# Kernel optimization log

Hardware: AMD Instinct MI355X
Metric: run time of the kernel (lower is better)

## Reference

```python
import jax, jax.numpy as jnp
import numpy as np

NUM_USERS = 100_000
NUM_ITEMS = 50_000
EMBED_DIM = 64
NUM_LAYERS = 3
NUM_BASE_EDGES = 2_000_000
BATCH = 4096


def setup_inputs() -> dict:
    key = jax.random.key(0)
    k_ue, k_ie, k_u, k_i, k_uid, k_iid = jax.random.split(key, 6)
    N = NUM_USERS + NUM_ITEMS
    # learned embedding tables (std=0.01 init as in the torch module)
    user_emb = 0.01 * jax.random.normal(k_ue, (NUM_USERS, EMBED_DIM), dtype=jnp.float32)
    item_emb = 0.01 * jax.random.normal(k_ie, (NUM_ITEMS, EMBED_DIM), dtype=jnp.float32)
    # random bipartite interaction edges (u, v); symmetrized as in _build_graph
    u = jax.random.randint(k_u, (NUM_BASE_EDGES,), 0, NUM_USERS, dtype=jnp.int32)
    v = jax.random.randint(k_i, (NUM_BASE_EDGES,), 0, NUM_ITEMS, dtype=jnp.int32) + NUM_USERS
    rows = jnp.concatenate([u, v])  # [2E]
    cols = jnp.concatenate([v, u])  # [2E]
    # symmetric degree normalization: A_hat[r,c] = 1 / (sqrt(deg[r]) * sqrt(deg[c]))
    deg = jax.ops.segment_sum(jnp.ones_like(rows, dtype=jnp.float32), rows, num_segments=N)
    sqrt_deg = jnp.sqrt(deg)
    vals = 1.0 / (sqrt_deg[rows] * sqrt_deg[cols])
    user_ids = jax.random.randint(k_uid, (BATCH,), 0, NUM_USERS, dtype=jnp.int32)
    item_ids = jax.random.randint(k_iid, (BATCH,), 0, NUM_ITEMS, dtype=jnp.int32)
    return {
        "user_emb": user_emb,
        "item_emb": item_emb,
        "vals": vals,
        "rows": rows,
        "cols": cols,
        "user_ids": user_ids,
        "item_ids": item_ids,
    }


def _spmm(vals, rows, cols, x, num_segments):
    # COO SpMM: out[r] += vals[e] * x[cols[e]]  (irregular gather + scatter-add)
    return jax.ops.segment_sum(vals[:, None] * x[cols], rows, num_segments=num_segments)


def reference(user_emb, item_emb, vals, rows, cols, user_ids, item_ids):
    num_users = user_emb.shape[0]
    N = num_users + item_emb.shape[0]
    all_emb = jnp.concatenate([user_emb, item_emb], axis=0)  # [N, D]
    acc = jnp.zeros_like(all_emb)
    for _ in range(NUM_LAYERS):  # eval mode: no stochastic noise injection
        all_emb = _spmm(vals, rows, cols, all_emb, N)
        acc = acc + all_emb
    final = acc / NUM_LAYERS  # mean over layer outputs
    u = final[user_ids]                       # [B, D]
    i = final[item_ids + num_users]           # [B, D]
    return (u * i).sum(axis=-1)               # [B]
```

## Files before the change

### kernel.cpp

```cpp
#include <hip/hip_runtime.h>


#define EMBED_DIM 64
#define NUM_LAYERS 3
#define RSHIFT 8
#define RMASK 255
#define NBMAX 640
#define CAPU 8192
#define CAPI 12288
#define TP 7168
#define OUT_CAP 12288

__device__ __forceinline__ int bucket_base(int b, int BSPLIT) {
    int lo = (b < BSPLIT) ? b : BSPLIT;
    int hi = (b > BSPLIT) ? (b - BSPLIT) : 0;
    return lo * CAPU + hi * CAPI;
}


__device__ __forceinline__ unsigned bf16pair(float a, float b) {
    unsigned ia = __float_as_uint(a);
    unsigned ib = __float_as_uint(b);
    ia = (ia + 0x7fffu + ((ia >> 16) & 1u)) >> 16;
    ib = (ib + 0x7fffu + ((ib >> 16) & 1u)) & 0xffff0000u;
    return ia | ib;
}
__device__ __forceinline__ float bf_lo(unsigned u) { return __uint_as_float(u << 16); }
__device__ __forceinline__ float bf_hi(unsigned u) { return __uint_as_float(u & 0xffff0000u); }


__global__ __launch_bounds__(1024) void split_kernel(const int* __restrict__ uu,
                                                     const int* __restrict__ vv,
                                                     int* __restrict__ gcur,
                                                     int* __restrict__ bin, int E2, int NB,
                                                     int BSPLIT) {
    __shared__ int h[NBMAX], exl[NBMAX], curb[NBMAX], gb[NBMAX];
    __shared__ int wp[16];
    __shared__ int stage[2 * TP];
    int tid = threadIdx.x;
    int lane = tid & 63, wid = tid >> 6;
    for (int i = tid; i < NB; i += 1024) h[i] = 0;
    __syncthreads();
    int e0 = blockIdx.x * TP, e1 = min(e0 + TP, E2);
    int j = e0 + tid * 4;
    for (; j + 3 < e1; j += 4096) {
        int4 u4 = *(const int4*)(uu + j);
        int4 v4 = *(const int4*)(vv + j);
        atomicAdd(&h[u4.x >> RSHIFT], 1); atomicAdd(&h[v4.x >> RSHIFT], 1);
        atomicAdd(&h[u4.y >> RSHIFT], 1); atomicAdd(&h[v4.y >> RSHIFT], 1);
        atomicAdd(&h[u4.z >> RSHIFT], 1); atomicAdd(&h[v4.z >> RSHIFT], 1);
        atomicAdd(&h[u4.w >> RSHIFT], 1); atomicAdd(&h[v4.w >> RSHIFT], 1);
    }
    for (; j < e1; ++j) {
        atomicAdd(&h[uu[j] >> RSHIFT], 1);
        atomicAdd(&h[vv[j] >> RSHIFT], 1);
    }
    __syncthreads();
    {
        int v0 = (tid < NB) ? h[tid] : 0;
        int x = v0;
        for (int off = 1; off < 64; off <<= 1) {
            int y = __shfl_up(x, off, 64);
            if (lane >= off) x += y;
        }
        if (lane == 63) wp[wid] = x;
        __syncthreads();
        int wadd = 0;
        for (int k = 0; k < wid; ++k) wadd += wp[k];
        if (tid < NB) exl[tid] = wadd + x - v0;
        __syncthreads();
    }
    for (int b = tid; b < NB; b += 1024) {
        curb[b] = exl[b];
        gb[b]   = h[b] ? (bucket_base(b, BSPLIT) + atomicAdd(&gcur[b], h[b])) : 0;
    }
    __syncthreads();
    j = e0 + tid * 4;
    for (; j + 3 < e1; j += 4096) {
        int4 u4 = *(const int4*)(uu + j);
        int4 v4 = *(const int4*)(vv + j);
        int p;
        p = atomicAdd(&curb[u4.x >> RSHIFT], 1); stage[p] = (v4.x << RSHIFT) | (u4.x & RMASK);
        p = atomicAdd(&curb[v4.x >> RSHIFT], 1); stage[p] = (u4.x << RSHIFT) | (v4.x & RMASK);
        p = atomicAdd(&curb[u4.y >> RSHIFT], 1); stage[p] = (v4.y << RSHIFT) | (u4.y & RMASK);
        p = atomicAdd(&curb[v4.y >> RSHIFT], 1); stage[p] = (u4.y << RSHIFT) | (v4.y & RMASK);
        p = atomicAdd(&curb[u4.z >> RSHIFT], 1); stage[p] = (v4.z << RSHIFT) | (u4.z & RMASK);
        p = atomicAdd(&curb[v4.z >> RSHIFT], 1); stage[p] = (u4.z << RSHIFT) | (v4.z & RMASK);
        p = atomicAdd(&curb[u4.w >> RSHIFT], 1); stage[p] = (v4.w << RSHIFT) | (u4.w & RMASK);
        p = atomicAdd(&curb[v4.w >> RSHIFT], 1); stage[p] = (u4.w << RSHIFT) | (v4.w & RMASK);
    }
    for (; j < e1; ++j) {
        int u = uu[j], v = vv[j];
        int p1 = atomicAdd(&curb[u >> RSHIFT], 1);
        stage[p1] = (v << RSHIFT) | (u & RMASK);
        int p2 = atomicAdd(&curb[v >> RSHIFT], 1);
        stage[p2] = (u << RSHIFT) | (v & RMASK);
    }
    __syncthreads();
    int noct = tid >> 3, osub = tid & 7;
    for (int b = noct; b < NB; b += 128) {
        int cnt_b = h[b];
        int st = exl[b], g = gb[b];
        for (int k = osub; k < cnt_b; k += 8) bin[g + k] = stage[st + k];
    }
}


__global__ __launch_bounds__(1024) void csr_kernel(const int* __restrict__ bin,
                                                   const int* __restrict__ gcur,
                                                   int2* __restrict__ rpd,
                                                   int* __restrict__ col_idx,
                                                   const float4* __restrict__ ue,
                                                   const float4* __restrict__ ie,
                                                   unsigned* __restrict__ w0x,
                                                   int N, int U, int BSPLIT, int NB) {
    __shared__ int h2[256], cur2[256];
    __shared__ float rs2[256];
    __shared__ int wp[16];
    __shared__ __align__(16) int outst[OUT_CAP];
    int nbi = NB - BSPLIT;
    int bb  = blockIdx.x;
    int b   = (bb < nbi) ? (BSPLIT + bb) : (bb - nbi);
    int tid = threadIdx.x;
    int lane = tid & 63, wid = tid >> 6;
    int s = bucket_base(b, BSPLIT);
    int cnt = gcur[b];
    if (tid < 256) h2[tid] = 0;
    __syncthreads();
    int cnt4 = cnt >> 2;
    const int4* bin4 = (const int4*)(bin + s);
    for (int j = tid; j < cnt4; j += 1024) {
        int4 v = bin4[j];
        atomicAdd(&h2[v.x & RMASK], 1);
        atomicAdd(&h2[v.y & RMASK], 1);
        atomicAdd(&h2[v.z & RMASK], 1);
        atomicAdd(&h2[v.w & RMASK], 1);
    }
    for (int j = (cnt4 << 2) + tid; j < cnt; j += 1024) atomicAdd(&h2[bin[s + j] & RMASK], 1);
    __syncthreads();
    int myh = (tid < 256) ? h2[tid] : 0;
    if (tid < 256) rs2[tid] = (myh > 0) ? rsqrtf((float)myh) : 0.0f;
    {
        int x = myh;
        for (int off = 1; off < 64; off <<= 1) {
            int y = __shfl_up(x, off, 64);
            if (lane >= off) x += y;
        }
        if (lane == 63) wp[wid] = x;
        __syncthreads();
        if (tid < 256) {
            int wadd = 0;
            for (int k = 0; k < wid; ++k) wadd += wp[k];
            cur2[tid] = wadd + x - myh;
        }
    }
    int gr = (b << RSHIFT) + tid;
    if (tid < 256 && gr < N) {
        int2 v; v.x = s + cur2[tid]; v.y = myh;
        rpd[gr] = v;
    }
    __syncthreads();
    if (cnt <= OUT_CAP) {
        for (int j = tid; j < cnt4; j += 1024) {
            int4 v = bin4[j];
            int p;
            p = atomicAdd(&cur2[v.x & RMASK], 1); outst[p] = v.x >> RSHIFT;
            p = atomicAdd(&cur2[v.y & RMASK], 1); outst[p] = v.y >> RSHIFT;
            p = atomicAdd(&cur2[v.z & RMASK], 1); outst[p] = v.z >> RSHIFT;
            p = atomicAdd(&cur2[v.w & RMASK], 1); outst[p] = v.w >> RSHIFT;
        }
        for (int j = (cnt4 << 2) + tid; j < cnt; j += 1024) {
            int v = bin[s + j];
            int p = atomicAdd(&cur2[v & RMASK], 1);
            outst[p] = v >> RSHIFT;
        }
        __syncthreads();
        int4* dst4 = (int4*)(col_idx + s);
        for (int j = tid; j < cnt4; j += 1024) dst4[j] = ((const int4*)outst)[j];
        for (int j = (cnt4 << 2) + tid; j < cnt; j += 1024) col_idx[s + j] = outst[j];
    } else {
        for (int j = tid; j < cnt; j += 1024) {
            int v = bin[s + j];
            int p = atomicAdd(&cur2[v & RMASK], 1);
            col_idx[s + p] = v >> RSHIFT;
        }
    }
    for (int idx = tid; idx < 256 * 16; idx += 1024) {
        int rl = idx >> 4, sub = idx & 15;
        int n = (b << RSHIFT) + rl;
        if (n < N) {
            float4 v = (n < U) ? ue[(size_t)n * 16 + sub] : ie[(size_t)(n - U) * 16 + sub];
            float rs = rs2[rl];
            uint2 o;
            o.x = bf16pair(v.x * rs, v.y * rs);
            o.y = bf16pair(v.z * rs, v.w * rs);
            ((uint2*)w0x)[(size_t)n * 16 + sub] = o;
        }
    }
}


__global__ __launch_bounds__(256) void spmm_kernel(const int2* __restrict__ rpd,
                                                   const int* __restrict__ col_idx,
                                                   const uint4* __restrict__ x4,
                                                   uint4* __restrict__ y4, int N) {
    int gw   = (blockIdx.x * blockDim.x + threadIdx.x) >> 6;
    int lane = threadIdx.x & 63;
    int oct  = lane >> 3, sub = lane & 7;
    int r = gw * 8 + oct;
    if (r >= N) return;
    int2 rd = rpd[r];
    int s = rd.x;
    int d = rd.y;
    float2 a0 = {0, 0}, a1 = {0, 0}, a2 = {0, 0}, a3 = {0, 0};
    int k = 0;
    for (; k + 3 < d; k += 4) {
        int c0 = col_idx[s + k];
        int c1 = col_idx[s + k + 1];
        int c2 = col_idx[s + k + 2];
        int c3 = col_idx[s + k + 3];
        uint4 u0 = x4[(size_t)c0 * 8 + sub];
        uint4 u1 = x4[(size_t)c1 * 8 + sub];
        uint4 u2 = x4[(size_t)c2 * 8 + sub];
        uint4 u3 = x4[(size_t)c3 * 8 + sub];
        a0.x += bf_lo(u0.x); a0.y += bf_hi(u0.x);
        a1.x += bf_lo(u0.y); a1.y += bf_hi(u0.y);
        a2.x += bf_lo(u0.z); a2.y += bf_hi(u0.z);
        a3.x += bf_lo(u0.w); a3.y += bf_hi(u0.w);
        a0.x += bf_lo(u1.x); a0.y += bf_hi(u1.x);
        a1.x += bf_lo(u1.y); a1.y += bf_hi(u1.y);
        a2.x += bf_lo(u1.z); a2.y += bf_hi(u1.z);
        a3.x += bf_lo(u1.w); a3.y += bf_hi(u1.w);
        a0.x += bf_lo(u2.x); a0.y += bf_hi(u2.x);
        a1.x += bf_lo(u2.y); a1.y += bf_hi(u2.y);
        a2.x += bf_lo(u2.z); a2.y += bf_hi(u2.z);
        a3.x += bf_lo(u2.w); a3.y += bf_hi(u2.w);
        a0.x += bf_lo(u3.x); a0.y += bf_hi(u3.x);
        a1.x += bf_lo(u3.y); a1.y += bf_hi(u3.y);
        a2.x += bf_lo(u3.z); a2.y += bf_hi(u3.z);
        a3.x += bf_lo(u3.w); a3.y += bf_hi(u3.w);
    }
    for (; k < d; ++k) {
        int c0 = col_idx[s + k];
        uint4 u0 = x4[(size_t)c0 * 8 + sub];
        a0.x += bf_lo(u0.x); a0.y += bf_hi(u0.x);
        a1.x += bf_lo(u0.y); a1.y += bf_hi(u0.y);
        a2.x += bf_lo(u0.z); a2.y += bf_hi(u0.z);
        a3.x += bf_lo(u0.w); a3.y += bf_hi(u0.w);
    }
    float inv = (d > 0) ? (1.0f / (float)d) : 0.0f;
    uint4 o;
    o.x = bf16pair(a0.x * inv, a0.y * inv);
    o.y = bf16pair(a1.x * inv, a1.y * inv);
    o.z = bf16pair(a2.x * inv, a2.y * inv);
    o.w = bf16pair(a3.x * inv, a3.y * inv);
    y4[(size_t)r * 8 + sub] = o;
}


__global__ __launch_bounds__(128) void batch_readout_kernel(const int2* __restrict__ rpd,
                                                            const int* __restrict__ col_idx,
                                                            const uint4* __restrict__ x4,
                                                            const uint4* __restrict__ l1,
                                                            const uint4* __restrict__ l2,
                                                            const int* __restrict__ user_ids,
                                                            const int* __restrict__ item_ids,
                                                            float* __restrict__ out,
                                                            int B, int U) {
    __shared__ float sm[8][8][8];
    __shared__ float dsm[8];
    int tid = threadIdx.x;
    int oct = tid >> 3, sub = tid & 7;
    int pair = oct & 7, is_item = oct >> 3;
    int b = blockIdx.x * 8 + pair;
    bool active = (b < B);
    float sv[8];
#pragma unroll
    for (int k = 0; k < 8; ++k) sv[k] = 0.0f;
    float dd = 0.0f;
    if (active) {
        int r = is_item ? (item_ids[b] + U) : user_ids[b];
        int2 rd = rpd[r];
        int s = rd.x;
        int d = rd.y;
        dd = (float)d;
        float2 a0 = {0, 0}, a1 = {0, 0}, a2 = {0, 0}, a3 = {0, 0};
        int k = 0;
        for (; k + 3 < d; k += 4) {
            int c0 = col_idx[s + k];
            int c1 = col_idx[s + k + 1];
            int c2 = col_idx[s + k + 2];
            int c3 = col_idx[s + k + 3];
            uint4 u0 = x4[(size_t)c0 * 8 + sub];
            uint4 u1 = x4[(size_t)c1 * 8 + sub];
            uint4 u2 = x4[(size_t)c2 * 8 + sub];
            uint4 u3 = x4[(size_t)c3 * 8 + sub];
            a0.x += bf_lo(u0.x); a0.y += bf_hi(u0.x);
            a1.x += bf_lo(u0.y); a1.y += bf_hi(u0.y);
            a2.x += bf_lo(u0.z); a2.y += bf_hi(u0.z);
            a3.x += bf_lo(u0.w); a3.y += bf_hi(u0.w);
            a0.x += bf_lo(u1.x); a0.y += bf_hi(u1.x);
            a1.x += bf_lo(u1.y); a1.y += bf_hi(u1.y);
            a2.x += bf_lo(u1.z); a2.y += bf_hi(u1.z);
            a3.x += bf_lo(u1.w); a3.y += bf_hi(u1.w);
            a0.x += bf_lo(u2.x); a0.y += bf_hi(u2.x);
            a1.x += bf_lo(u2.y); a1.y += bf_hi(u2.y);
            a2.x += bf_lo(u2.z); a2.y += bf_hi(u2.z);
            a3.x += bf_lo(u2.w); a3.y += bf_hi(u2.w);
            a0.x += bf_lo(u3.x); a0.y += bf_hi(u3.x);
            a1.x += bf_lo(u3.y); a1.y += bf_hi(u3.y);
            a2.x += bf_lo(u3.z); a2.y += bf_hi(u3.z);
            a3.x += bf_lo(u3.w); a3.y += bf_hi(u3.w);
        }
        for (; k < d; ++k) {
            int c0 = col_idx[s + k];
            uint4 u0 = x4[(size_t)c0 * 8 + sub];
            a0.x += bf_lo(u0.x); a0.y += bf_hi(u0.x);
            a1.x += bf_lo(u0.y); a1.y += bf_hi(u0.y);
            a2.x += bf_lo(u0.z); a2.y += bf_hi(u0.z);
            a3.x += bf_lo(u0.w); a3.y += bf_hi(u0.w);
        }
        float inv = (d > 0) ? (1.0f / (float)d) : 0.0f;
        uint4 u1v = l1[(size_t)r * 8 + sub];
        uint4 u2v = l2[(size_t)r * 8 + sub];
        sv[0] = bf_lo(u1v.x) + bf_lo(u2v.x) + a0.x * inv;
        sv[1] = bf_hi(u1v.x) + bf_hi(u2v.x) + a0.y * inv;
        sv[2] = bf_lo(u1v.y) + bf_lo(u2v.y) + a1.x * inv;
        sv[3] = bf_hi(u1v.y) + bf_hi(u2v.y) + a1.y * inv;
        sv[4] = bf_lo(u1v.z) + bf_lo(u2v.z) + a2.x * inv;
        sv[5] = bf_hi(u1v.z) + bf_hi(u2v.z) + a2.y * inv;
        sv[6] = bf_lo(u1v.w) + bf_lo(u2v.w) + a3.x * inv;
        sv[7] = bf_hi(u1v.w) + bf_hi(u2v.w) + a3.y * inv;
    }
    if (is_item) {
#pragma unroll
        for (int k = 0; k < 8; ++k) sm[pair][sub][k] = sv[k];
        if (sub == 0) dsm[pair] = dd;
    }
    __syncthreads();
    if (!is_item && active) {
        float p = 0.0f;
#pragma unroll
        for (int k = 0; k < 8; ++k) p += sv[k] * sm[pair][sub][k];
#pragma unroll
        for (int off = 4; off > 0; off >>= 1) p += __shfl_down(p, off, 8);
        if (sub == 0) {
            float du = dd;
            float di = dsm[pair];
            out[b] = p * sqrtf(du) * sqrtf(di) * (1.0f / (NUM_LAYERS * NUM_LAYERS));
        }
    }
}


extern "C" void kernel_launch(void* const* d_in, const int* in_sizes, int n_in,
                              void* d_out, int out_size, void* d_ws, size_t ws_size,
                              hipStream_t stream) {
    const float* user_emb = (const float*)d_in[0];
    const float* item_emb = (const float*)d_in[1];
    const int*   rows     = (const int*)d_in[3];
    const int*   cols     = (const int*)d_in[4];
    const int*   user_ids = (const int*)d_in[5];
    const int*   item_ids = (const int*)d_in[6];
    float*       out      = (float*)d_out;

    const int U = in_sizes[0] / EMBED_DIM;
    const int I = in_sizes[1] / EMBED_DIM;
    const int E2 = in_sizes[3] >> 1;
    const int B = in_sizes[5];
    const int N = U + I;
    const int NB = (N + RMASK) >> RSHIFT;
    const int BSPLIT = U >> RSHIFT;

    const long long TOT = (long long)((NB < BSPLIT ? NB : BSPLIT)) * CAPU +
                          (long long)((NB > BSPLIT) ? (NB - BSPLIT) : 0) * CAPI;

    char* w = (char*)d_ws;
    unsigned* x2      = (unsigned*)w; w += (size_t)N * 32 * sizeof(unsigned);
    unsigned* L1      = (unsigned*)w; w += (size_t)N * 32 * sizeof(unsigned);
    unsigned* L2      = (unsigned*)w; w += (size_t)N * 32 * sizeof(unsigned);
    int*      bin     = (int*)w;      w += (size_t)TOT * sizeof(int);
    int*      col_idx = (int*)w;      w += (size_t)TOT * sizeof(int);
    int2*     rpd     = (int2*)w;     w += (size_t)N * sizeof(int2);
    int*      gcur    = (int*)w;      w += (size_t)NB * sizeof(int);

    const int GP = (E2 + TP - 1) / TP;

    hipMemsetAsync(gcur, 0, (size_t)NB * sizeof(int), stream);
    split_kernel<<<GP, 1024, 0, stream>>>(rows, cols, gcur, bin, E2, NB, BSPLIT);
    csr_kernel<<<NB, 1024, 0, stream>>>(bin, gcur, rpd, col_idx,
                                        (const float4*)user_emb, (const float4*)item_emb,
                                        x2, N, U, BSPLIT, NB);

    const int T = 256;
    const int GS = (N * 8 + T - 1) / T;
    spmm_kernel<<<GS, T, 0, stream>>>(rpd, col_idx, (const uint4*)x2, (uint4*)L1, N);
    spmm_kernel<<<GS, T, 0, stream>>>(rpd, col_idx, (const uint4*)L1, (uint4*)L2, N);

    batch_readout_kernel<<<(B + 7) / 8, 128, 0, stream>>>(rpd, col_idx,
                                                          (const uint4*)L2,
                                                          (const uint4*)L1, (const uint4*)L2,
                                                          user_ids, item_ids, out, B, U);
}
```

Measured before the change: 283.7 us.

## Split bf16 embedding tables into two 64-byte column halves for SpMM gathers

Stores each layer's bf16 embeddings as two separate half-width arrays (32 dims each, 64 bytes per row) instead of one 128-byte row. The SpMM kernel now assigns 4 lanes per row per half and interleaves blocks across the two halves, so each pass gathers from a table half the size, which should make the working set fit better in cache. The trade-off is that every col_idx is read twice (once per half), and rows from the two halves are handled by different blocks.

```diff
diff --git a/kernel.cpp b/kernel.cpp
--- a/kernel.cpp
+++ b/kernel.cpp
@@ -112,7 +112,8 @@
                                                    int* __restrict__ col_idx,
                                                    const float4* __restrict__ ue,
                                                    const float4* __restrict__ ie,
-                                                   unsigned* __restrict__ w0x,
+                                                   unsigned* __restrict__ w0a,
+                                                   unsigned* __restrict__ w0b,
                                                    int N, int U, int BSPLIT, int NB) {
     __shared__ int h2[256], cur2[256];
     __shared__ float rs2[256];
@@ -194,7 +195,8 @@
             uint2 o;
             o.x = bf16pair(v.x * rs, v.y * rs);
             o.y = bf16pair(v.z * rs, v.w * rs);
-            ((uint2*)w0x)[(size_t)n * 16 + sub] = o;
+            unsigned* dst = (sub < 8) ? w0a : w0b;
+            ((uint2*)dst)[(size_t)n * 8 + (sub & 7)] = o;
         }
     }
 }
@@ -202,13 +204,19 @@
 
 __global__ __launch_bounds__(256) void spmm_kernel(const int2* __restrict__ rpd,
                                                    const int* __restrict__ col_idx,
-                                                   const uint4* __restrict__ x4,
-                                                   uint4* __restrict__ y4, int N) {
-    int gw   = (blockIdx.x * blockDim.x + threadIdx.x) >> 6;
-    int lane = threadIdx.x & 63;
-    int oct  = lane >> 3, sub = lane & 7;
-    int r = gw * 8 + oct;
+                                                   const uint4* __restrict__ xa,
+                                                   const uint4* __restrict__ xb,
+                                                   uint4* __restrict__ ya,
+                                                   uint4* __restrict__ yb, int N) {
+    int bid = blockIdx.x;
+    int xm = bid & 7, jm = bid >> 3;
+    int half = xm >> 2;
+    int gidx = jm * 4 + (xm & 3);
+    int quad = threadIdx.x >> 2, sub = threadIdx.x & 3;
+    int r = gidx * 64 + quad;
     if (r >= N) return;
+    const uint4* xs = half ? xb : xa;
+    uint4*       ys = half ? yb : ya;
     int2 rd = rpd[r];
     int s = rd.x;
     int d = rd.y;
@@ -219,10 +227,10 @@
         int c1 = col_idx[s + k + 1];
         int c2 = col_idx[s + k + 2];
         int c3 = col_idx[s + k + 3];
-        uint4 u0 = x4[(size_t)c0 * 8 + sub];
-        uint4 u1 = x4[(size_t)c1 * 8 + sub];
-        uint4 u2 = x4[(size_t)c2 * 8 + sub];
-        uint4 u3 = x4[(size_t)c3 * 8 + sub];
+        uint4 u0 = xs[(size_t)c0 * 4 + sub];
+        uint4 u1 = xs[(size_t)c1 * 4 + sub];
+        uint4 u2 = xs[(size_t)c2 * 4 + sub];
+        uint4 u3 = xs[(size_t)c3 * 4 + sub];
         a0.x += bf_lo(u0.x); a0.y += bf_hi(u0.x);
         a1.x += bf_lo(u0.y); a1.y += bf_hi(u0.y);
         a2.x += bf_lo(u0.z); a2.y += bf_hi(u0.z);
@@ -242,7 +250,7 @@
     }
     for (; k < d; ++k) {
         int c0 = col_idx[s + k];
-        uint4 u0 = x4[(size_t)c0 * 8 + sub];
+        uint4 u0 = xs[(size_t)c0 * 4 + sub];
         a0.x += bf_lo(u0.x); a0.y += bf_hi(u0.x);
         a1.x += bf_lo(u0.y); a1.y += bf_hi(u0.y);
         a2.x += bf_lo(u0.z); a2.y += bf_hi(u0.z);
@@ -254,15 +262,16 @@
     o.y = bf16pair(a1.x * inv, a1.y * inv);
     o.z = bf16pair(a2.x * inv, a2.y * inv);
     o.w = bf16pair(a3.x * inv, a3.y * inv);
-    y4[(size_t)r * 8 + sub] = o;
+    ys[(size_t)r * 4 + sub] = o;
 }
 
 
 __global__ __launch_bounds__(128) void batch_readout_kernel(const int2* __restrict__ rpd,
                                                             const int* __restrict__ col_idx,
-                                                            const uint4* __restrict__ x4,
-                                                            const uint4* __restrict__ l1,
-                                                            const uint4* __restrict__ l2,
+                                                            const uint4* __restrict__ l2a,
+                                                            const uint4* __restrict__ l2b,
+                                                            const uint4* __restrict__ l1a,
+                                                            const uint4* __restrict__ l1b,
                                                             const int* __restrict__ user_ids,
                                                             const int* __restrict__ item_ids,
                                                             float* __restrict__ out,
@@ -274,6 +283,9 @@
     int pair = oct & 7, is_item = oct >> 3;
     int b = blockIdx.x * 8 + pair;
     bool active = (b < B);
+    const uint4* g2 = (sub < 4) ? l2a : l2b;
+    const uint4* g1 = (sub < 4) ? l1a : l1b;
+    int ssub = sub & 3;
     float sv[8];
 #pragma unroll
     for (int k = 0; k < 8; ++k) sv[k] = 0.0f;
@@ -291,10 +303,10 @@
             int c1 = col_idx[s + k + 1];
             int c2 = col_idx[s + k + 2];
             int c3 = col_idx[s + k + 3];
-            uint4 u0 = x4[(size_t)c0 * 8 + sub];
-            uint4 u1 = x4[(size_t)c1 * 8 + sub];
-            uint4 u2 = x4[(size_t)c2 * 8 + sub];
-            uint4 u3 = x4[(size_t)c3 * 8 + sub];
+            uint4 u0 = g2[(size_t)c0 * 4 + ssub];
+            uint4 u1 = g2[(size_t)c1 * 4 + ssub];
+            uint4 u2 = g2[(size_t)c2 * 4 + ssub];
+            uint4 u3 = g2[(size_t)c3 * 4 + ssub];
             a0.x += bf_lo(u0.x); a0.y += bf_hi(u0.x);
             a1.x += bf_lo(u0.y); a1.y += bf_hi(u0.y);
             a2.x += bf_lo(u0.z); a2.y += bf_hi(u0.z);
@@ -314,15 +326,15 @@
         }
         for (; k < d; ++k) {
             int c0 = col_idx[s + k];
-            uint4 u0 = x4[(size_t)c0 * 8 + sub];
+            uint4 u0 = g2[(size_t)c0 * 4 + ssub];
             a0.x += bf_lo(u0.x); a0.y += bf_hi(u0.x);
             a1.x += bf_lo(u0.y); a1.y += bf_hi(u0.y);
             a2.x += bf_lo(u0.z); a2.y += bf_hi(u0.z);
             a3.x += bf_lo(u0.w); a3.y += bf_hi(u0.w);
         }
         float inv = (d > 0) ? (1.0f / (float)d) : 0.0f;
-        uint4 u1v = l1[(size_t)r * 8 + sub];
-        uint4 u2v = l2[(size_t)r * 8 + sub];
+        uint4 u1v = g1[(size_t)r * 4 + ssub];
+        uint4 u2v = g2[(size_t)r * 4 + ssub];
         sv[0] = bf_lo(u1v.x) + bf_lo(u2v.x) + a0.x * inv;
         sv[1] = bf_hi(u1v.x) + bf_hi(u2v.x) + a0.y * inv;
         sv[2] = bf_lo(u1v.y) + bf_lo(u2v.y) + a1.x * inv;
@@ -376,13 +388,16 @@
                           (long long)((NB > BSPLIT) ? (NB - BSPLIT) : 0) * CAPI;
 
     char* w = (char*)d_ws;
-    unsigned* x2      = (unsigned*)w; w += (size_t)N * 32 * sizeof(unsigned);
-    unsigned* L1      = (unsigned*)w; w += (size_t)N * 32 * sizeof(unsigned);
-    unsigned* L2      = (unsigned*)w; w += (size_t)N * 32 * sizeof(unsigned);
-    int*      bin     = (int*)w;      w += (size_t)TOT * sizeof(int);
-    int*      col_idx = (int*)w;      w += (size_t)TOT * sizeof(int);
-    int2*     rpd     = (int2*)w;     w += (size_t)N * sizeof(int2);
-    int*      gcur    = (int*)w;      w += (size_t)NB * sizeof(int);
+    unsigned* x2a = (unsigned*)w; w += (size_t)N * 16 * sizeof(unsigned);
+    unsigned* x2b = (unsigned*)w; w += (size_t)N * 16 * sizeof(unsigned);
+    unsigned* L1a = (unsigned*)w; w += (size_t)N * 16 * sizeof(unsigned);
+    unsigned* L1b = (unsigned*)w; w += (size_t)N * 16 * sizeof(unsigned);
+    unsigned* L2a = (unsigned*)w; w += (size_t)N * 16 * sizeof(unsigned);
+    unsigned* L2b = (unsigned*)w; w += (size_t)N * 16 * sizeof(unsigned);
+    int*      bin     = (int*)w;  w += (size_t)TOT * sizeof(int);
+    int*      col_idx = (int*)w;  w += (size_t)TOT * sizeof(int);
+    int2*     rpd     = (int2*)w; w += (size_t)N * sizeof(int2);
+    int*      gcur    = (int*)w;  w += (size_t)NB * sizeof(int);
 
     const int GP = (E2 + TP - 1) / TP;
 
@@ -390,15 +405,20 @@
     split_kernel<<<GP, 1024, 0, stream>>>(rows, cols, gcur, bin, E2, NB, BSPLIT);
     csr_kernel<<<NB, 1024, 0, stream>>>(bin, gcur, rpd, col_idx,
                                         (const float4*)user_emb, (const float4*)item_emb,
-                                        x2, N, U, BSPLIT, NB);
-
-    const int T = 256;
-    const int GS = (N * 8 + T - 1) / T;
-    spmm_kernel<<<GS, T, 0, stream>>>(rpd, col_idx, (const uint4*)x2, (uint4*)L1, N);
-    spmm_kernel<<<GS, T, 0, stream>>>(rpd, col_idx, (const uint4*)L1, (uint4*)L2, N);
+                                        x2a, x2b, N, U, BSPLIT, NB);
+
+    const int NG = (N + 63) >> 6;
+    const int GB = (NG + 3) >> 2;
+    const int GRID = GB * 8;
+    spmm_kernel<<<GRID, 256, 0, stream>>>(rpd, col_idx,
+                                          (const uint4*)x2a, (const uint4*)x2b,
+                                          (uint4*)L1a, (uint4*)L1b, N);
+    spmm_kernel<<<GRID, 256, 0, stream>>>(rpd, col_idx,
+                                          (const uint4*)L1a, (const uint4*)L1b,
+                                          (uint4*)L2a, (uint4*)L2b, N);
 
     batch_readout_kernel<<<(B + 7) / 8, 128, 0, stream>>>(rpd, col_idx,
-                                                          (const uint4*)L2,
-                                                          (const uint4*)L1, (const uint4*)L2,
+                                                          (const uint4*)L2a, (const uint4*)L2b,
+                                                          (const uint4*)L1a, (const uint4*)L1b,
                                                           user_ids, item_ids, out, B, U);
 }
```

Result: slower. 334.3 us (+17.8%).
